# Kernel optimization log

Hardware: AMD Instinct MI355X
Metric: run time of the kernel (lower is better)

Reference implementation:

```python
import jax, jax.numpy as jnp
import numpy as np

H, DK, DV = 16, 64, 64
DECAY = 0.99
WRITE_STRENGTH = 1.0


def setup_inputs() -> dict:
    key = jax.random.key(0)
    ks = jax.random.split(key, 7)
    B, S, D = 4, 4096, 2048
    sd = 1.0 / np.sqrt(D)
    return {
        "hidden": jax.random.normal(ks[0], (B, S, D), jnp.float32),
        "memory": jax.random.normal(ks[1], (H, DK, DV), jnp.float32) * 0.02,
        "Wk": jax.random.normal(ks[2], (H * DK, D), jnp.float32) * sd,
        "Wv": jax.random.normal(ks[3], (H * DV, D), jnp.float32) * sd,
        "Wq": jax.random.normal(ks[4], (H * DK, D), jnp.float32) * sd,
        "Wg": jax.random.normal(ks[5], (D, D), jnp.float32) * sd,
        "Wo": jax.random.normal(ks[6], (D, H * DV), jnp.float32) * (1.0 / np.sqrt(H * DV)),
    }


def reference(hidden, memory, Wk, Wv, Wq, Wg, Wo):
    B, S, D = hidden.shape
    # projections (Linear, bias=False): x @ W^T
    k = (hidden @ Wk.T).reshape(B, S, H, DK)
    v = (hidden @ Wv.T).reshape(B, S, H, DV)
    q = (hidden @ Wq.T).reshape(B, S, H, DK)
    # read with pre-update memory: r = q^T M
    readout = jnp.einsum('bshk,hkv->bshv', q, memory).reshape(B, S, H * DV)
    # output gate: h' = h + sigmoid(Wg h) * (Wo r)
    gate = jax.nn.sigmoid(hidden @ Wg.T)
    out = hidden + gate * (readout @ Wo.T)
    # decaying outer-product write: M' = lambda*M + rho * sum_i k_i v_i^T
    new_memory = DECAY * memory + WRITE_STRENGTH * jnp.einsum('bshk,bshv->hkv', k, v)
    return out, new_memory
```

## Files before the change

kernel.cpp:

```cpp
#include <hip/hip_runtime.h>
#include <hip/hip_bf16.h>

typedef __attribute__((ext_vector_type(4))) float f32x4;
typedef __bf16 bf16x8 __attribute__((ext_vector_type(8)));
typedef int int4v __attribute__((ext_vector_type(4)));

#define TOKENS 16384
#define DIM    2048
#define NKVQ   3072

__device__ __forceinline__ void gload_lds16(const void* g, void* l) {
  __builtin_amdgcn_global_load_lds((const __attribute__((address_space(1))) void*)g,
                                   (__attribute__((address_space(3))) void*)l, 16, 0, 0);
}

__global__ void cast8_kernel(const float* __restrict__ src, __bf16* __restrict__ dst, int n8) {
  int i = blockIdx.x * blockDim.x + threadIdx.x;
  if (i >= n8) return;
  const float4* s = (const float4*)src;
  float4 a = s[2 * i], b = s[2 * i + 1];
  bf16x8 o;
  o[0] = (__bf16)a.x; o[1] = (__bf16)a.y; o[2] = (__bf16)a.z; o[3] = (__bf16)a.w;
  o[4] = (__bf16)b.x; o[5] = (__bf16)b.y; o[6] = (__bf16)b.z; o[7] = (__bf16)b.w;
  ((bf16x8*)dst)[i] = o;
}

__global__ void weff_kernel(const float* __restrict__ Wo, const float* __restrict__ mem,
                            __bf16* __restrict__ Weff) {
  int idx = blockIdx.x * blockDim.x + threadIdx.x;
  int d = idx >> 10, hk = idx & 1023, h = hk >> 6;
  const float* wo = Wo + d * 1024 + h * 64;
  const float* mm = mem + hk * 64;
  float s = 0.f;
  #pragma unroll 8
  for (int v = 0; v < 64; ++v) s += wo[v] * mm[v];
  Weff[idx] = (__bf16)s;
}

__device__ __forceinline__ void gemm256_core(
    const __bf16* __restrict__ A, int lda,
    const __bf16* __restrict__ B, int ldb,
    int m0, int n0, int nt, char* sm, f32x4 acc[8][4]) {

  const int tid = threadIdx.x, lane = tid & 63, wid = tid >> 6;
  const int wr = wid >> 2, wc = wid & 3;
  const int lrow = lane & 15, kc = lane >> 4, s7 = lrow & 7;

  const int rowA = (wr * 64 + lrow) * 128;
  const int rowB = (wc * 32 + lrow) * 128 + 32768;
  const int sw0 = ((0 + kc) ^ s7) << 4;
  const int sw1 = ((4 + kc) ^ s7) << 4;

  unsigned oa[2][2], ob[2][2];
  #pragma unroll
  for (int h = 0; h < 2; ++h)
    #pragma unroll
    for (int L = 0; L < 2; ++L) {
      int l = h * 1024 + L * 512 + tid;
      int rl = l >> 3;
      int c  = (l & 7) ^ (rl & 7);
      int ra = ((rl & 127) >> 6) * 128 + h * 64 + (rl & 63);
      int rb = ((rl & 127) >> 5) * 64  + h * 32 + (rl & 31);
      oa[h][L] = (unsigned)(((m0 + ra) * lda + c * 8) * 2);
      ob[h][L] = (unsigned)(((n0 + rb) * ldb + c * 8) * 2);
    }
  const char* Ab = (const char*)A;
  const char* Bb = (const char*)B;

  bf16x8 avA[4][2], avB[4][2], bvA[2][2], bvB[2][2];

#define BARX() asm volatile("s_barrier" ::: "memory")
#define VM2()  asm volatile("s_waitcnt vmcnt(2)" ::: "memory")
#define VM0()  asm volatile("s_waitcnt vmcnt(0)" ::: "memory")
#define STA(bb, h, tt) do { \
    gload_lds16(Ab + oa[h][0] + (tt) * 128, sm + (bb) * 65536 + ((h) * 1024 + tid) * 16); \
    gload_lds16(Ab + oa[h][1] + (tt) * 128, sm + (bb) * 65536 + ((h) * 1024 + 512 + tid) * 16); } while (0)
#define STB(bb, h, tt) do { \
    gload_lds16(Bb + ob[h][0] + (tt) * 128, sm + (bb) * 65536 + 32768 + ((h) * 1024 + tid) * 16); \
    gload_lds16(Bb + ob[h][1] + (tt) * 128, sm + (bb) * 65536 + 32768 + ((h) * 1024 + 512 + tid) * 16); } while (0)
#define RD_AV(dst, bb, mh) \
    _Pragma("unroll") for (int f = 0; f < 4; ++f) { \
      dst[f][0] = *(const bf16x8*)(sm + (bb) * 65536 + (mh) * 16384 + rowA + f * 2048 + sw0); \
      dst[f][1] = *(const bf16x8*)(sm + (bb) * 65536 + (mh) * 16384 + rowA + f * 2048 + sw1); }
#define RD_BV(dst, bb, nh) \
    _Pragma("unroll") for (int n = 0; n < 2; ++n) { \
      dst[n][0] = *(const bf16x8*)(sm + (bb) * 65536 + (nh) * 16384 + rowB + n * 2048 + sw0); \
      dst[n][1] = *(const bf16x8*)(sm + (bb) * 65536 + (nh) * 16384 + rowB + n * 2048 + sw1); }
#define MM(av, bv, fo, no) do { \
    __builtin_amdgcn_s_setprio(1); \
    _Pragma("unroll") for (int f = 0; f < 4; ++f) \
      _Pragma("unroll") for (int n = 0; n < 2; ++n) { \
        acc[(fo) + f][(no) + n] = __builtin_amdgcn_mfma_f32_16x16x32_bf16(av[f][0], bv[n][0], acc[(fo) + f][(no) + n], 0, 0, 0); \
        acc[(fo) + f][(no) + n] = __builtin_amdgcn_mfma_f32_16x16x32_bf16(av[f][1], bv[n][1], acc[(fo) + f][(no) + n], 0, 0, 0); } \
    __builtin_amdgcn_s_setprio(0); } while (0)

#define TILE_PH(c, d, t) do { \
    RD_AV(avA, c, 0); RD_BV(bvA, c, 0); \
    STA(d, 0, (t) + 1); \
    BARX(); \
    MM(avA, bvA, 0, 0); \
    VM2(); BARX(); \
    RD_BV(bvB, c, 1); \
    STA(d, 1, (t) + 1); \
    BARX(); \
    MM(avA, bvB, 0, 2); \
    BARX(); \
    RD_AV(avB, c, 1); \
    STB(d, 0, (t) + 1); \
    BARX(); \
    MM(avB, bvB, 4, 2); \
    BARX(); \
    STB(d, 1, (t) + 1); \
    BARX(); \
    MM(avB, bvA, 4, 0); \
    VM2(); BARX(); } while (0)

#define TILE_TAIL(c) do { \
    RD_AV(avA, c, 0); RD_BV(bvA, c, 0); \
    BARX(); \
    MM(avA, bvA, 0, 0); \
    VM0(); \
    RD_BV(bvB, c, 1); \
    MM(avA, bvB, 0, 2); \
    RD_AV(avB, c, 1); \
    MM(avB, bvB, 4, 2); \
    MM(avB, bvA, 4, 0); } while (0)

  STA(0, 0, 0); STA(0, 1, 0); STB(0, 0, 0); STB(0, 1, 0);
  VM2(); BARX();

  for (int i = 0, e = (nt - 2) >> 1; i < e; ++i) {
    const int t = i << 1;
    TILE_PH(0, 1, t);
    TILE_PH(1, 0, t + 1);
  }
  TILE_PH(0, 1, nt - 2);
  TILE_TAIL(1);
#undef TILE_PH
#undef TILE_TAIL
#undef MM
#undef RD_AV
#undef RD_BV
#undef STA
#undef STB
#undef BARX
#undef VM2
#undef VM0
}

__global__ void __launch_bounds__(512, 1)
gemm_fused_kernel(const __bf16* __restrict__ Xb, const __bf16* __restrict__ W1,
                  __bf16* __restrict__ Y, __bf16* __restrict__ Gb) {
  __shared__ __attribute__((aligned(16))) char smem[131072];
  const int x = blockIdx.x & 7;
  const int l = blockIdx.x >> 3;
  const int bm = x * 8 + (l & 7);
  const int bn = l >> 3;
  const int m0 = bm * 256, n0 = bn * 256;
  f32x4 acc[8][4] = {};
  gemm256_core(Xb, DIM, W1, DIM, m0, n0, 32, smem, acc);

  __syncthreads();
  const int tid = threadIdx.x, wid = tid >> 6, lane = tid & 63;
  const int wr = wid >> 2, wc = wid & 3;
  const int crow = (lane >> 4) << 2, ccol = lane & 15;
  const bool isY = bn < 12;
  #pragma unroll
  for (int f = 0; f < 8; ++f)
    #pragma unroll
    for (int n = 0; n < 4; ++n)
      #pragma unroll
      for (int j = 0; j < 4; ++j) {
        int r = wr * 128 + f * 16 + crow + j;
        int c = wc * 64 + n * 16 + ccol;
        float v = acc[f][n][j];
        if (!isY) v = 1.0f / (1.0f + __expf(-v));
        *(__bf16*)(smem + r * 512 + ((c * 2) ^ ((r & 7) << 4))) = (__bf16)v;
      }
  __syncthreads();
  const int rsub = tid >> 5, ch = tid & 31;
  if (isY) {
    #pragma unroll
    for (int p = 0; p < 16; ++p) {
      int r = p * 16 + rsub;
      bf16x8 v = *(const bf16x8*)(smem + r * 512 + ((ch * 16) ^ ((r & 7) << 4)));
      __builtin_nontemporal_store(__builtin_bit_cast(int4v, v),
          (int4v*)(Y + (size_t)(m0 + r) * NKVQ + n0 + ch * 8));
    }
  } else {
    const int c0 = n0 - 3072;
    #pragma unroll
    for (int p = 0; p < 16; ++p) {
      int r = p * 16 + rsub;
      bf16x8 v = *(const bf16x8*)(smem + r * 512 + ((ch * 16) ^ ((r & 7) << 4)));
      __builtin_nontemporal_store(__builtin_bit_cast(int4v, v),
          (int4v*)(Gb + (size_t)(m0 + r) * DIM + c0 + ch * 8));
    }
  }
}

__global__ void __launch_bounds__(512, 1)
gemm_read_kernel(const __bf16* __restrict__ Yq, const __bf16* __restrict__ Weff,
                 const __bf16* __restrict__ Gb, const float* __restrict__ hidden,
                 float* __restrict__ out) {
  __shared__ __attribute__((aligned(16))) char smem[131072];
  const int x = blockIdx.x & 7;
  const int l = blockIdx.x >> 3;
  const int bm = x * 8 + (l & 7);
  const int bn = l >> 3;
  const int m0 = bm * 256, n0 = bn * 256;
  f32x4 acc[8][4] = {};
  gemm256_core(Yq, NKVQ, Weff, 1024, m0, n0, 16, smem, acc);

  const int tid = threadIdx.x, wid = tid >> 6, lane = tid & 63;
  const int wr = wid >> 2, wc = wid & 3;
  const int crow = (lane >> 4) << 2, ccol = lane & 15;
  #pragma unroll
  for (int f = 0; f < 8; ++f) {
    int row = m0 + wr * 128 + f * 16 + crow;
    #pragma unroll
    for (int n = 0; n < 4; ++n) {
      int col = n0 + wc * 64 + n * 16 + ccol;
      #pragma unroll
      for (int j = 0; j < 4; ++j) {
        size_t idx = (size_t)(row + j) * DIM + col;
        out[idx] = hidden[idx] + (float)Gb[idx] * acc[f][n][j];
      }
    }
  }
}

__global__ void __launch_bounds__(256)
mem_update_kernel(const __bf16* __restrict__ Y, float* __restrict__ part) {
  const int h = blockIdx.x & 15, sp = blockIdx.x >> 4;
  __shared__ __attribute__((aligned(16))) __bf16 KT[64 * 32];
  __shared__ __attribute__((aligned(16))) __bf16 VT[64 * 32];
  const int tid = threadIdx.x, wid = tid >> 6, lane = tid & 63;
  const int lrow = lane & 15, lk = (lane >> 4) * 8;
  const __bf16* Kbase = Y + (size_t)sp * 1024 * NKVQ + h * 64;
  const __bf16* Vbase = Kbase + 1024;
  f32x4 acc[4] = {};
  const int t = tid >> 3, c8 = (tid & 7) * 8;
  for (int t0 = 0; t0 < 1024; t0 += 32) {
    __syncthreads();
    bf16x8 kv = *(const bf16x8*)(Kbase + (size_t)(t0 + t) * NKVQ + c8);
    bf16x8 vv = *(const bf16x8*)(Vbase + (size_t)(t0 + t) * NKVQ + c8);
    #pragma unroll
    for (int j = 0; j < 8; ++j) {
      KT[(c8 + j) * 32 + t] = kv[j];
      VT[(c8 + j) * 32 + t] = vv[j];
    }
    __syncthreads();
    bf16x8 af = *(const bf16x8*)(KT + (wid * 16 + lrow) * 32 + lk);
    #pragma unroll
    for (int n = 0; n < 4; ++n) {
      bf16x8 bf_ = *(const bf16x8*)(VT + (n * 16 + lrow) * 32 + lk);
      acc[n] = __builtin_amdgcn_mfma_f32_16x16x32_bf16(af, bf_, acc[n], 0, 0, 0);
    }
  }
  float* pp = part + ((size_t)sp * 16 + h) * 4096;
  const int crow = wid * 16 + (lane >> 4) * 4, ccol = lane & 15;
  #pragma unroll
  for (int n = 0; n < 4; ++n)
    #pragma unroll
    for (int r = 0; r < 4; ++r)
      pp[(crow + r) * 64 + n * 16 + ccol] = acc[n][r];
}

__global__ void mem_reduce_kernel(const float* __restrict__ part, const float* __restrict__ mem,
                                  float* __restrict__ out) {
  int i = blockIdx.x * blockDim.x + threadIdx.x;
  float s = 0.99f * mem[i];
  #pragma unroll
  for (int sp = 0; sp < 16; ++sp) s += part[sp * 65536 + i];
  out[i] = s;
}

extern "C" void kernel_launch(void* const* d_in, const int* in_sizes, int n_in,
                              void* d_out, int out_size, void* d_ws, size_t ws_size,
                              hipStream_t stream) {
  const float* hidden = (const float*)d_in[0];
  const float* memory = (const float*)d_in[1];
  const float* Wk = (const float*)d_in[2];
  const float* Wv = (const float*)d_in[3];
  const float* Wq = (const float*)d_in[4];
  const float* Wg = (const float*)d_in[5];
  const float* Wo = (const float*)d_in[6];
  float* out = (float*)d_out;
  float* mem_out = out + (size_t)TOKENS * DIM;

  char* ws = (char*)d_ws;
  __bf16* Xb   = (__bf16*)(ws);
  __bf16* W1   = (__bf16*)(ws + 67108864);
  __bf16* Weff = (__bf16*)(ws + 88080384);
  __bf16* Yb   = (__bf16*)(ws + 92274688);
  __bf16* Gb   = (__bf16*)(ws + 192937984);
  float*  part = (float*)(ws + 260046848);

  cast8_kernel<<<16384, 256, 0, stream>>>(hidden, Xb, 4194304);
  cast8_kernel<<<1024, 256, 0, stream>>>(Wk, W1, 262144);
  cast8_kernel<<<1024, 256, 0, stream>>>(Wv, W1 + 2097152, 262144);
  cast8_kernel<<<1024, 256, 0, stream>>>(Wq, W1 + 4194304, 262144);
  cast8_kernel<<<2048, 256, 0, stream>>>(Wg, W1 + 6291456, 524288);
  weff_kernel<<<8192, 256, 0, stream>>>(Wo, memory, Weff);

  gemm_fused_kernel<<<1280, 512, 0, stream>>>(Xb, W1, Yb, Gb);
  gemm_read_kernel<<<512, 512, 0, stream>>>(Yb + 2048, Weff, Gb, hidden, out);

  mem_update_kernel<<<256, 256, 0, stream>>>(Yb, part);
  mem_reduce_kernel<<<256, 256, 0, stream>>>(part, memory, mem_out);
}
```

Baseline: 605.9 us.

## Fold Wq into readout weights and compute memory update via Gram matrix

The query projection is folded into the effective readout weights (Weff·Wq). Those weights are interleaved with Wg so that one GEMM over hidden yields both the gate pre-activation and the readout projection, and the output epilogue applies sigmoid and the residual directly. The memory write is rewritten as Wk·(XᵀX)·Wvᵀ: a split-K Gram-matrix GEMM over a transposed bf16 copy of hidden, followed by small reductions and a per-head MFMA kernel. This removes the materialized K/V/Q and gate buffers and the second readout GEMM. In exchange it adds a full 2048×2048×16384 Gram GEMM, a hidden transpose, fp32 partial buffers, and extra bf16 rounding of intermediate products.

```diff
diff --git a/kernel.cpp b/kernel.cpp
--- a/kernel.cpp
+++ b/kernel.cpp
@@ -3,11 +3,11 @@
 
 typedef __attribute__((ext_vector_type(4))) float f32x4;
 typedef __bf16 bf16x8 __attribute__((ext_vector_type(8)));
+typedef __bf16 bf16x4 __attribute__((ext_vector_type(4)));
 typedef int int4v __attribute__((ext_vector_type(4)));
 
 #define TOKENS 16384
 #define DIM    2048
-#define NKVQ   3072
 
 __device__ __forceinline__ void gload_lds16(const void* g, void* l) {
   __builtin_amdgcn_global_load_lds((const __attribute__((address_space(1))) void*)g,
@@ -23,6 +23,68 @@
   o[0] = (__bf16)a.x; o[1] = (__bf16)a.y; o[2] = (__bf16)a.z; o[3] = (__bf16)a.w;
   o[4] = (__bf16)b.x; o[5] = (__bf16)b.y; o[6] = (__bf16)b.z; o[7] = (__bf16)b.w;
   ((bf16x8*)dst)[i] = o;
+}
+
+__global__ void castWg_inter_kernel(const float* __restrict__ Wg, __bf16* __restrict__ W1) {
+  int i = blockIdx.x * blockDim.x + threadIdx.x;
+  int g = i >> 8, c8 = (i & 255) * 8;
+  const float4* s = (const float4*)(Wg + (size_t)g * DIM + c8);
+  float4 a = s[0], b = s[1];
+  bf16x8 o;
+  o[0] = (__bf16)a.x; o[1] = (__bf16)a.y; o[2] = (__bf16)a.z; o[3] = (__bf16)a.w;
+  o[4] = (__bf16)b.x; o[5] = (__bf16)b.y; o[6] = (__bf16)b.z; o[7] = (__bf16)b.w;
+  int r = 32 * (g >> 4) + (g & 15);
+  *(bf16x8*)(W1 + (size_t)r * DIM + c8) = o;
+}
+
+__global__ void __launch_bounds__(256)
+transcast_kernel(const float* __restrict__ src, __bf16* __restrict__ Xb, __bf16* __restrict__ XT) {
+  __shared__ __bf16 Ts[64][68];
+  const int ti = blockIdx.x >> 5, di = blockIdx.x & 31;
+  const int s0 = ti << 6, d0 = di << 6;
+  const int t = threadIdx.x, r0 = t >> 4, c4 = t & 15;
+  #pragma unroll
+  for (int i = 0; i < 4; ++i) {
+    int row = r0 + i * 16;
+    float4 v = *(const float4*)(src + (size_t)(s0 + row) * DIM + d0 + c4 * 4);
+    bf16x4 o; o[0] = (__bf16)v.x; o[1] = (__bf16)v.y; o[2] = (__bf16)v.z; o[3] = (__bf16)v.w;
+    *(bf16x4*)(Xb + (size_t)(s0 + row) * DIM + d0 + c4 * 4) = o;
+    Ts[row][c4 * 4 + 0] = o[0]; Ts[row][c4 * 4 + 1] = o[1];
+    Ts[row][c4 * 4 + 2] = o[2]; Ts[row][c4 * 4 + 3] = o[3];
+  }
+  __syncthreads();
+  const int d = t >> 2, sq = t & 3;
+  #pragma unroll
+  for (int g = 0; g < 2; ++g) {
+    bf16x8 o;
+    #pragma unroll
+    for (int k = 0; k < 8; ++k) o[k] = Ts[sq * 16 + g * 8 + k][d];
+    *(bf16x8*)(XT + (size_t)(d0 + d) * TOKENS + s0 + sq * 16 + g * 8) = o;
+  }
+}
+
+__global__ void __launch_bounds__(256)
+transWq_kernel(const float* __restrict__ Wq, __bf16* __restrict__ WqT) {
+  __shared__ __bf16 Ts[64][68];
+  const int ti = blockIdx.x >> 5, di = blockIdx.x & 31;
+  const int h0 = ti << 6, d0 = di << 6;
+  const int t = threadIdx.x, r0 = t >> 4, c4 = t & 15;
+  #pragma unroll
+  for (int i = 0; i < 4; ++i) {
+    int row = r0 + i * 16;
+    float4 v = *(const float4*)(Wq + (size_t)(h0 + row) * DIM + d0 + c4 * 4);
+    Ts[row][c4 * 4 + 0] = (__bf16)v.x; Ts[row][c4 * 4 + 1] = (__bf16)v.y;
+    Ts[row][c4 * 4 + 2] = (__bf16)v.z; Ts[row][c4 * 4 + 3] = (__bf16)v.w;
+  }
+  __syncthreads();
+  const int d = t >> 2, sq = t & 3;
+  #pragma unroll
+  for (int g = 0; g < 2; ++g) {
+    bf16x8 o;
+    #pragma unroll
+    for (int k = 0; k < 8; ++k) o[k] = Ts[sq * 16 + g * 8 + k][d];
+    *(bf16x8*)(WqT + (size_t)(d0 + d) * 1024 + h0 + sq * 16 + g * 8) = o;
+  }
 }
 
 __global__ void weff_kernel(const float* __restrict__ Wo, const float* __restrict__ mem,
@@ -149,8 +211,144 @@
 }
 
 __global__ void __launch_bounds__(512, 1)
-gemm_fused_kernel(const __bf16* __restrict__ Xb, const __bf16* __restrict__ W1,
-                  __bf16* __restrict__ Y, __bf16* __restrict__ Gb) {
+w2_kernel(const __bf16* __restrict__ Weff, const __bf16* __restrict__ WqT,
+          __bf16* __restrict__ W1) {
+  __shared__ __attribute__((aligned(16))) char smem[131072];
+  const int bm = blockIdx.x >> 3, bn = blockIdx.x & 7;
+  const int m0 = bm * 256, n0 = bn * 256;
+  f32x4 acc[8][4] = {};
+  gemm256_core(Weff, 1024, WqT, 1024, m0, n0, 16, smem, acc);
+
+  const int tid = threadIdx.x, wid = tid >> 6, lane = tid & 63;
+  const int wr = wid >> 2, wc = wid & 3;
+  const int crow = (lane >> 4) << 2, ccol = lane & 15;
+  #pragma unroll
+  for (int f = 0; f < 8; ++f) {
+    int base16 = (m0 + wr * 128) >> 4;
+    #pragma unroll
+    for (int n = 0; n < 4; ++n) {
+      int col = n0 + wc * 64 + n * 16 + ccol;
+      #pragma unroll
+      for (int j = 0; j < 4; ++j) {
+        int r = 32 * (base16 + f) + 16 + crow + j;
+        W1[(size_t)r * DIM + col] = (__bf16)acc[f][n][j];
+      }
+    }
+  }
+}
+
+__global__ void __launch_bounds__(512, 1)
+g_kernel(const __bf16* __restrict__ XT, float* __restrict__ Gpart) {
+  __shared__ __attribute__((aligned(16))) char smem[131072];
+  const int ks = blockIdx.x >> 6, rr = blockIdx.x & 63;
+  const int bm = rr >> 3, bn = rr & 7;
+  const int m0 = bm * 256, n0 = bn * 256;
+  const __bf16* Xk = XT + ks * 4096;
+  f32x4 acc[8][4] = {};
+  gemm256_core(Xk, TOKENS, Xk, TOKENS, m0, n0, 64, smem, acc);
+
+  float* P = Gpart + (size_t)ks * 4194304;
+  const int tid = threadIdx.x, wid = tid >> 6, lane = tid & 63;
+  const int wr = wid >> 2, wc = wid & 3;
+  const int crow = (lane >> 4) << 2, ccol = lane & 15;
+  #pragma unroll
+  for (int f = 0; f < 8; ++f) {
+    int row = m0 + wr * 128 + f * 16 + crow;
+    #pragma unroll
+    for (int n = 0; n < 4; ++n) {
+      int col = n0 + wc * 64 + n * 16 + ccol;
+      #pragma unroll
+      for (int j = 0; j < 4; ++j)
+        P[(size_t)(row + j) * DIM + col] = acc[f][n][j];
+    }
+  }
+}
+
+__global__ void greduce_kernel(const float* __restrict__ Gpart, __bf16* __restrict__ Gb16) {
+  int i4 = blockIdx.x * blockDim.x + threadIdx.x;
+  float4 s = ((const float4*)Gpart)[i4];
+  #pragma unroll
+  for (int k = 1; k < 4; ++k) {
+    float4 p = ((const float4*)(Gpart + (size_t)k * 4194304))[i4];
+    s.x += p.x; s.y += p.y; s.z += p.z; s.w += p.w;
+  }
+  bf16x4 o; o[0] = (__bf16)s.x; o[1] = (__bf16)s.y; o[2] = (__bf16)s.z; o[3] = (__bf16)s.w;
+  ((bf16x4*)Gb16)[i4] = o;
+}
+
+__global__ void __launch_bounds__(512, 1)
+wkg_kernel(const __bf16* __restrict__ Wkb, const __bf16* __restrict__ Gb16,
+           float* __restrict__ WkGpart) {
+  __shared__ __attribute__((aligned(16))) char smem[131072];
+  const int ks = blockIdx.x >> 5, rr = blockIdx.x & 31;
+  const int bm = rr >> 3, bn = rr & 7;
+  const int m0 = bm * 256, n0 = bn * 256;
+  f32x4 acc[8][4] = {};
+  gemm256_core(Wkb + ks * 512, DIM, Gb16 + ks * 512, DIM, m0, n0, 8, smem, acc);
+
+  float* P = WkGpart + (size_t)ks * 2097152;
+  const int tid = threadIdx.x, wid = tid >> 6, lane = tid & 63;
+  const int wr = wid >> 2, wc = wid & 3;
+  const int crow = (lane >> 4) << 2, ccol = lane & 15;
+  #pragma unroll
+  for (int f = 0; f < 8; ++f) {
+    int row = m0 + wr * 128 + f * 16 + crow;
+    #pragma unroll
+    for (int n = 0; n < 4; ++n) {
+      int col = n0 + wc * 64 + n * 16 + ccol;
+      #pragma unroll
+      for (int j = 0; j < 4; ++j)
+        P[(size_t)(row + j) * DIM + col] = acc[f][n][j];
+    }
+  }
+}
+
+__global__ void wkgreduce_kernel(const float* __restrict__ WkGpart, __bf16* __restrict__ WkG) {
+  int i4 = blockIdx.x * blockDim.x + threadIdx.x;
+  float4 s = ((const float4*)WkGpart)[i4];
+  #pragma unroll
+  for (int k = 1; k < 4; ++k) {
+    float4 p = ((const float4*)(WkGpart + (size_t)k * 2097152))[i4];
+    s.x += p.x; s.y += p.y; s.z += p.z; s.w += p.w;
+  }
+  bf16x4 o; o[0] = (__bf16)s.x; o[1] = (__bf16)s.y; o[2] = (__bf16)s.z; o[3] = (__bf16)s.w;
+  ((bf16x4*)WkG)[i4] = o;
+}
+
+__global__ void __launch_bounds__(256)
+memfinal_kernel(const __bf16* __restrict__ WkG, const __bf16* __restrict__ Wvb,
+                const float* __restrict__ mem, float* __restrict__ mem_out) {
+  const int h = blockIdx.x;
+  const int tid = threadIdx.x, lane = tid & 63, w = tid >> 6;
+  const int lrow = lane & 15, kc = lane >> 4;
+  const __bf16* Ah = WkG + (size_t)h * 64 * DIM;
+  const __bf16* Bh = Wvb + (size_t)h * 64 * DIM;
+  f32x4 acc[4] = {};
+  const int arow = (w * 16 + lrow) * DIM + kc * 8;
+  #pragma unroll 2
+  for (int kt = 0; kt < 64; ++kt) {
+    int ko = kt * 32;
+    bf16x8 a = *(const bf16x8*)(Ah + arow + ko);
+    #pragma unroll
+    for (int n = 0; n < 4; ++n) {
+      bf16x8 b = *(const bf16x8*)(Bh + (n * 16 + lrow) * DIM + kc * 8 + ko);
+      acc[n] = __builtin_amdgcn_mfma_f32_16x16x32_bf16(a, b, acc[n], 0, 0, 0);
+    }
+  }
+  const int crow = (lane >> 4) * 4, ccol = lane & 15;
+  const int base = h * 4096;
+  #pragma unroll
+  for (int n = 0; n < 4; ++n)
+    #pragma unroll
+    for (int j = 0; j < 4; ++j) {
+      int idx = base + (w * 16 + crow + j) * 64 + n * 16 + ccol;
+      mem_out[idx] = 0.99f * mem[idx] + acc[n][j];
+    }
+}
+
+__global__ void __launch_bounds__(512, 1)
+gemm_main_kernel(const __bf16* __restrict__ Xb, const __bf16* __restrict__ W1,
+                 const float* __restrict__ hidden, float* __restrict__ out) {
   __shared__ __attribute__((aligned(16))) char smem[131072];
   const int x = blockIdx.x & 7;
   const int l = blockIdx.x >> 3;
@@ -160,120 +358,23 @@
   f32x4 acc[8][4] = {};
   gemm256_core(Xb, DIM, W1, DIM, m0, n0, 32, smem, acc);
 
-  __syncthreads();
   const int tid = threadIdx.x, wid = tid >> 6, lane = tid & 63;
   const int wr = wid >> 2, wc = wid & 3;
   const int crow = (lane >> 4) << 2, ccol = lane & 15;
-  const bool isY = bn < 12;
-  #pragma unroll
-  for (int f = 0; f < 8; ++f)
-    #pragma unroll
-    for (int n = 0; n < 4; ++n)
-      #pragma unroll
-      for (int j = 0; j < 4; ++j) {
-        int r = wr * 128 + f * 16 + crow + j;
-        int c = wc * 64 + n * 16 + ccol;
-        float v = acc[f][n][j];
-        if (!isY) v = 1.0f / (1.0f + __expf(-v));
-        *(__bf16*)(smem + r * 512 + ((c * 2) ^ ((r & 7) << 4))) = (__bf16)v;
-      }
-  __syncthreads();
-  const int rsub = tid >> 5, ch = tid & 31;
-  if (isY) {
-    #pragma unroll
-    for (int p = 0; p < 16; ++p) {
-      int r = p * 16 + rsub;
-      bf16x8 v = *(const bf16x8*)(smem + r * 512 + ((ch * 16) ^ ((r & 7) << 4)));
-      __builtin_nontemporal_store(__builtin_bit_cast(int4v, v),
-          (int4v*)(Y + (size_t)(m0 + r) * NKVQ + n0 + ch * 8));
-    }
-  } else {
-    const int c0 = n0 - 3072;
-    #pragma unroll
-    for (int p = 0; p < 16; ++p) {
-      int r = p * 16 + rsub;
-      bf16x8 v = *(const bf16x8*)(smem + r * 512 + ((ch * 16) ^ ((r & 7) << 4)));
-      __builtin_nontemporal_store(__builtin_bit_cast(int4v, v),
-          (int4v*)(Gb + (size_t)(m0 + r) * DIM + c0 + ch * 8));
-    }
-  }
-}
-
-__global__ void __launch_bounds__(512, 1)
-gemm_read_kernel(const __bf16* __restrict__ Yq, const __bf16* __restrict__ Weff,
-                 const __bf16* __restrict__ Gb, const float* __restrict__ hidden,
-                 float* __restrict__ out) {
-  __shared__ __attribute__((aligned(16))) char smem[131072];
-  const int x = blockIdx.x & 7;
-  const int l = blockIdx.x >> 3;
-  const int bm = x * 8 + (l & 7);
-  const int bn = l >> 3;
-  const int m0 = bm * 256, n0 = bn * 256;
-  f32x4 acc[8][4] = {};
-  gemm256_core(Yq, NKVQ, Weff, 1024, m0, n0, 16, smem, acc);
-
-  const int tid = threadIdx.x, wid = tid >> 6, lane = tid & 63;
-  const int wr = wid >> 2, wc = wid & 3;
-  const int crow = (lane >> 4) << 2, ccol = lane & 15;
   #pragma unroll
   for (int f = 0; f < 8; ++f) {
     int row = m0 + wr * 128 + f * 16 + crow;
     #pragma unroll
-    for (int n = 0; n < 4; ++n) {
-      int col = n0 + wc * 64 + n * 16 + ccol;
+    for (int np = 0; np < 2; ++np) {
+      int col = (n0 >> 1) + wc * 32 + np * 16 + ccol;
       #pragma unroll
       for (int j = 0; j < 4; ++j) {
         size_t idx = (size_t)(row + j) * DIM + col;
-        out[idx] = hidden[idx] + (float)Gb[idx] * acc[f][n][j];
+        float gv = 1.0f / (1.0f + __expf(-acc[f][2 * np][j]));
+        out[idx] = hidden[idx] + gv * acc[f][2 * np + 1][j];
       }
     }
   }
-}
-
-__global__ void __launch_bounds__(256)
-mem_update_kernel(const __bf16* __restrict__ Y, float* __restrict__ part) {
-  const int h = blockIdx.x & 15, sp = blockIdx.x >> 4;
-  __shared__ __attribute__((aligned(16))) __bf16 KT[64 * 32];
-  __shared__ __attribute__((aligned(16))) __bf16 VT[64 * 32];
-  const int tid = threadIdx.x, wid = tid >> 6, lane = tid & 63;
-  const int lrow = lane & 15, lk = (lane >> 4) * 8;
-  const __bf16* Kbase = Y + (size_t)sp * 1024 * NKVQ + h * 64;
-  const __bf16* Vbase = Kbase + 1024;
-  f32x4 acc[4] = {};
-  const int t = tid >> 3, c8 = (tid & 7) * 8;
-  for (int t0 = 0; t0 < 1024; t0 += 32) {
-    __syncthreads();
-    bf16x8 kv = *(const bf16x8*)(Kbase + (size_t)(t0 + t) * NKVQ + c8);
-    bf16x8 vv = *(const bf16x8*)(Vbase + (size_t)(t0 + t) * NKVQ + c8);
-    #pragma unroll
-    for (int j = 0; j < 8; ++j) {
-      KT[(c8 + j) * 32 + t] = kv[j];
-      VT[(c8 + j) * 32 + t] = vv[j];
-    }
-    __syncthreads();
-    bf16x8 af = *(const bf16x8*)(KT + (wid * 16 + lrow) * 32 + lk);
-    #pragma unroll
-    for (int n = 0; n < 4; ++n) {
-      bf16x8 bf_ = *(const bf16x8*)(VT + (n * 16 + lrow) * 32 + lk);
-      acc[n] = __builtin_amdgcn_mfma_f32_16x16x32_bf16(af, bf_, acc[n], 0, 0, 0);
-    }
-  }
-  float* pp = part + ((size_t)sp * 16 + h) * 4096;
-  const int crow = wid * 16 + (lane >> 4) * 4, ccol = lane & 15;
-  #pragma unroll
-  for (int n = 0; n < 4; ++n)
-    #pragma unroll
-    for (int r = 0; r < 4; ++r)
-      pp[(crow + r) * 64 + n * 16 + ccol] = acc[n][r];
-}
-
-__global__ void mem_reduce_kernel(const float* __restrict__ part, const float* __restrict__ mem,
-                                  float* __restrict__ out) {
-  int i = blockIdx.x * blockDim.x + threadIdx.x;
-  float s = 0.99f * mem[i];
-  #pragma unroll
-  for (int sp = 0; sp < 16; ++sp) s += part[sp * 65536 + i];
-  out[i] = s;
 }
 
 extern "C" void kernel_launch(void* const* d_in, const int* in_sizes, int n_in,
@@ -291,22 +392,33 @@
 
   char* ws = (char*)d_ws;
   __bf16* Xb   = (__bf16*)(ws);
-  __bf16* W1   = (__bf16*)(ws + 67108864);
-  __bf16* Weff = (__bf16*)(ws + 88080384);
-  __bf16* Yb   = (__bf16*)(ws + 92274688);
-  __bf16* Gb   = (__bf16*)(ws + 192937984);
-  float*  part = (float*)(ws + 260046848);
-
-  cast8_kernel<<<16384, 256, 0, stream>>>(hidden, Xb, 4194304);
-  cast8_kernel<<<1024, 256, 0, stream>>>(Wk, W1, 262144);
-  cast8_kernel<<<1024, 256, 0, stream>>>(Wv, W1 + 2097152, 262144);
-  cast8_kernel<<<1024, 256, 0, stream>>>(Wq, W1 + 4194304, 262144);
-  cast8_kernel<<<2048, 256, 0, stream>>>(Wg, W1 + 6291456, 524288);
+  __bf16* XT   = (__bf16*)(ws + 67108864);
+  __bf16* W1   = (__bf16*)(ws + 134217728);
+  __bf16* Wkb  = (__bf16*)(ws + 150994944);
+  __bf16* Wvb  = (__bf16*)(ws + 155189248);
+  __bf16* Weff = (__bf16*)(ws + 159383552);
+  __bf16* WqT  = (__bf16*)(ws + 163577856);
+  __bf16* Gb16 = (__bf16*)(ws + 167772160);
+  __bf16* WkG  = (__bf16*)(ws + 176160768);
+  float*  Gpart   = (float*)(ws + 180355072);
+  float*  WkGpart = (float*)(ws + 180355072);
+
+  transcast_kernel<<<8192, 256, 0, stream>>>(hidden, Xb, XT);
+  castWg_inter_kernel<<<2048, 256, 0, stream>>>(Wg, W1);
+  cast8_kernel<<<1024, 256, 0, stream>>>(Wk, Wkb, 262144);
+  cast8_kernel<<<1024, 256, 0, stream>>>(Wv, Wvb, 262144);
   weff_kernel<<<8192, 256, 0, stream>>>(Wo, memory, Weff);
-
-  gemm_fused_kernel<<<1280, 512, 0, stream>>>(Xb, W1, Yb, Gb);
-  gemm_read_kernel<<<512, 512, 0, stream>>>(Yb + 2048, Weff, Gb, hidden, out);
-
-  mem_update_kernel<<<256, 256, 0, stream>>>(Yb, part);
-  mem_reduce_kernel<<<256, 256, 0, stream>>>(part, memory, mem_out);
-}
+  transWq_kernel<<<512, 256, 0, stream>>>(Wq, WqT);
+
+  w2_kernel<<<64, 512, 0, stream>>>(Weff, WqT, W1);
+
+  g_kernel<<<256, 512, 0, stream>>>(XT, Gpart);
+  greduce_kernel<<<4096, 256, 0, stream>>>(Gpart, Gb16);
+
+  wkg_kernel<<<128, 512, 0, stream>>>(Wkb, Gb16, WkGpart);
+  wkgreduce_kernel<<<2048, 256, 0, stream>>>(WkGpart, WkG);
+
+  memfinal_kernel<<<16, 256, 0, stream>>>(WkG, Wvb, memory, mem_out);
+
+  gemm_main_kernel<<<1024, 512, 0, stream>>>(Xb, W1, hidden, out);
+}
```

New measurement: 639.0 us. 5.5% more time.
